# Kernel tuning notes

Measured on AMD Instinct MI355X. Metric: run time of the kernel, lower is better.

Reference implementation:

```python
import jax, jax.numpy as jnp
import numpy as np

D = 128          # fine voxel grid resolution
N0 = 250000
D_IN, D_BASE, D_OUT = 16, 8, 8
EPS = 1e-5
# (cin, cout) for conv0..conv6, conv7, conv9, conv11
_CH = [(16, 8), (8, 16), (16, 16), (16, 32), (32, 32), (32, 64), (64, 64), (64, 32), (32, 16), (16, 8)]

def _offsets():
    r = np.arange(-1, 2)
    return np.stack(np.meshgrid(r, r, r, indexing='ij'), -1).reshape(-1, 3)  # [27,3]

def _lookup_fn(coords, d):
    keys = (coords[:, 0].astype(np.int64) * d + coords[:, 1]) * d + coords[:, 2]
    order = np.argsort(keys)
    skeys = keys[order]
    def lookup(q):
        valid = ((q >= 0) & (q < d)).all(-1)
        k = (q[:, 0].astype(np.int64) * d + q[:, 1]) * d + q[:, 2]
        pos = np.clip(np.searchsorted(skeys, k), 0, len(skeys) - 1)
        return np.where(valid & (skeys[pos] == k), order[pos], -1).astype(np.int32)
    return lookup

def _nbr_same(coords, d):
    # stride-1 sparse conv: outputs at input coords, neighbors at coord+k
    lk = _lookup_fn(coords, d)
    return np.stack([lk(coords + o) for o in _offsets()], 1)  # [N,27]

def _nbr_down(c_out, c_in, d_in):
    # stride-2 conv: output p gathers inputs at 2p+k
    lk = _lookup_fn(c_in, d_in)
    return np.stack([lk(c_out * 2 + o) for o in _offsets()], 1)

def _nbr_up(c_out, c_in, d_in):
    # transposed stride-2 conv: output q gathers input p=(q-k)/2 where divisible
    lk = _lookup_fn(c_in, d_in)
    cols = []
    for o in _offsets():
        q = c_out - o
        div = (q % 2 == 0).all(-1)
        cols.append(np.where(div, lk(q // 2), -1).astype(np.int32))
    return np.stack(cols, 1)

def setup_inputs():
    rng = np.random.default_rng(0)
    flat = rng.choice(D ** 3, size=N0, replace=False)
    c0 = np.stack([flat // (D * D), (flat // D) % D, flat % D], 1).astype(np.int32)
    c1 = np.unique(c0 // 2, axis=0)
    c2 = np.unique(c1 // 2, axis=0)
    c3 = np.unique(c2 // 2, axis=0)
    inp = {
        'feats': jax.random.normal(jax.random.key(0), (N0, D_IN), jnp.float32),
        'nbr0': jnp.asarray(_nbr_same(c0, D)),
        'nbr_d01': jnp.asarray(_nbr_down(c1, c0, D)),
        'nbr1': jnp.asarray(_nbr_same(c1, D // 2)),
        'nbr_d12': jnp.asarray(_nbr_down(c2, c1, D // 2)),
        'nbr2': jnp.asarray(_nbr_same(c2, D // 4)),
        'nbr_d23': jnp.asarray(_nbr_down(c3, c2, D // 4)),
        'nbr3': jnp.asarray(_nbr_same(c3, D // 8)),
        'nbr_u32': jnp.asarray(_nbr_up(c2, c3, D // 8)),
        'nbr_u21': jnp.asarray(_nbr_up(c1, c2, D // 4)),
        'nbr_u10': jnp.asarray(_nbr_up(c0, c1, D // 2)),
    }
    key = jax.random.key(1)
    for i, (ci, co) in enumerate(_CH):
        key, kw = jax.random.split(key)
        inp['w%d' % i] = jax.random.normal(kw, (27, ci, co), jnp.float32) / np.sqrt(27.0 * ci)
        inp['g%d' % i] = jnp.ones((co,), jnp.float32)
        inp['b%d' % i] = jnp.zeros((co,), jnp.float32)
    inp['lin_w'] = jax.random.normal(jax.random.key(2), (D_OUT, D_BASE), jnp.float32) / np.sqrt(D_BASE)
    return inp

def _sconv_bn_relu(f, nbr, w, g, b):
    # f: [Nin,Cin], nbr: [Nout,27] (-1 = no neighbor), w: [27,Cin,Cout]
    gth = jnp.where((nbr >= 0)[..., None], f[jnp.maximum(nbr, 0)], 0.0)  # [Nout,27,Cin]
    y = jnp.einsum('nkc,kco->no', gth, w)
    mu = y.mean(0)                       # training-mode BatchNorm over active voxels
    var = y.var(0)
    return jax.nn.relu((y - mu) * jax.lax.rsqrt(var + EPS) * g + b)

def reference(feats, nbr0, nbr_d01, nbr1, nbr_d12, nbr2, nbr_d23, nbr3, nbr_u32, nbr_u21, nbr_u10,
              w0, g0, b0, w1, g1, b1, w2, g2, b2, w3, g3, b3, w4, g4, b4,
              w5, g5, b5, w6, g6, b6, w7, g7, b7, w8, g8, b8, w9, g9, b9, lin_w):
    c0f = _sconv_bn_relu(feats, nbr0, w0, g0, b0)
    c2f = _sconv_bn_relu(_sconv_bn_relu(c0f, nbr_d01, w1, g1, b1), nbr1, w2, g2, b2)
    c4f = _sconv_bn_relu(_sconv_bn_relu(c2f, nbr_d12, w3, g3, b3), nbr2, w4, g4, b4)
    x = _sconv_bn_relu(_sconv_bn_relu(c4f, nbr_d23, w5, g5, b5), nbr3, w6, g6, b6)
    x = c4f + _sconv_bn_relu(x, nbr_u32, w7, g7, b7)
    x = c2f + _sconv_bn_relu(x, nbr_u21, w8, g8, b8)
    x = c0f + _sconv_bn_relu(x, nbr_u10, w9, g9, b9)
    return x @ lin_w.T, x
```

## Files before the change

### kernel.cpp

```cpp
#include <hip/hip_runtime.h>

#define EPSV 1e-5f
#define NBUCKET 64

typedef __attribute__((ext_vector_type(8))) short short8;
typedef __attribute__((ext_vector_type(4))) float float4v;

static inline int cdiv(int a, int b) { return (a + b - 1) / b; }
static inline int imin(int a, int b) { return a < b ? a : b; }

__device__ inline unsigned short f2bf(float x) {
  unsigned u = __float_as_uint(x);
  return (unsigned short)((u + 0x7FFFu + ((u >> 16) & 1u)) >> 16);
}
__device__ inline float bf2f(unsigned short u) {
  return __uint_as_float(((unsigned)u) << 16);
}

struct PrepArgs {
  const float* w[10];
  unsigned short* wt[10];
  int ci[10];
  int co[10];
  int wcum[11];
  const float* feats;
  unsigned short* featsb;
  int nfeat4;
  float* stats;
};

__global__ __launch_bounds__(256) void prep_kernel(PrepArgs p, long total) {
  const int nstat4 = 10 * NBUCKET * 128 / 4;
  for (long tid0 = (long)blockIdx.x * 256 + threadIdx.x; tid0 < total;
       tid0 += (long)gridDim.x * 256) {
    long tid = tid0;
    if (tid < nstat4) {
      ((float4*)p.stats)[tid] = make_float4(0.f, 0.f, 0.f, 0.f);
      continue;
    }
    tid -= nstat4;
    if (tid < p.nfeat4) {
      float4 v = ((const float4*)p.feats)[tid];
      ushort4 r;
      r.x = f2bf(v.x); r.y = f2bf(v.y); r.z = f2bf(v.z); r.w = f2bf(v.w);
      ((ushort4*)p.featsb)[tid] = r;
      continue;
    }
    tid -= p.nfeat4;
    if (tid >= p.wcum[10]) continue;
    int i = 0;
    while (tid >= p.wcum[i + 1]) ++i;
    int e = (int)(tid - p.wcum[i]);
    int ci = p.ci[i], co = p.co[i];
    int k = e / (ci * co);
    int r = e - k * (ci * co);
    int o = r / ci;
    int c = r - o * ci;
    p.wt[i][((long)k * co + o) * ci + c] = f2bf(p.w[i][((long)k * ci + c) * co + o]);
  }
}

template<int CI, int CO, int MINW>
__global__ __launch_bounds__(256, MINW) void conv_mfma(
    const unsigned short* __restrict__ f, const int* __restrict__ nbr,
    const unsigned short* __restrict__ wt, unsigned short* __restrict__ y,
    float* __restrict__ stats, int nout) {
  constexpr int NCHUNK = (CI == 8) ? 7 : (CI == 16) ? 14 : (CI == 32) ? 27 : 54;
  constexpr int CIP = (CI == 64) ? 64 : (CI == 32) ? 40 : (CI == 16) ? 24 : 12;
  constexpr int RB = (CO < 16) ? CO : 16;
  constexpr bool TWO = (CI <= 16);
  constexpr int NT = TWO ? 2 : 1;

  __shared__ int nbrT[NT * 64 * 27];
  __shared__ unsigned short Bs[27 * RB * CIP];

  const int tid = threadIdx.x;
  const int lane = tid & 63;
  const int wid = tid >> 6;
  const int m = lane & 15;
  const int mm = m & (RB - 1);
  const int quad = lane >> 4;
  const int cbase = blockIdx.y * 16;
  const int co = cbase + m;
  const bool cok = co < CO;

  auto tapof = [&](int c) -> int {
    if constexpr (CI == 8) return c * 4 + quad;
    else if constexpr (CI == 16) return c * 2 + (quad >> 1);
    else if constexpr (CI == 32) return c;
    else return c >> 1;
  };
  auto cioof = [&](int c) -> int {
    if constexpr (CI == 8) return 0;
    else if constexpr (CI == 16) return (quad & 1) * 8;
    else if constexpr (CI == 32) return quad * 8;
    else return ((c & 1) << 5) + quad * 8;
  };
  auto baddr = [&](int tap, int r, int cio) -> int {
    if constexpr (CI == 64) {
      int byt = (tap * 16 + r) * 128 + cio * 2;
      byt ^= (r & 7) << 4;
      return byt >> 1;
    } else {
      return (tap * RB + r) * CIP + cio;
    }
  };

  const int rowb0 = blockIdx.x * (NT * 64);

  {
    constexpr int NC8 = CI / 8;
    for (int t = tid; t < 27 * RB * NC8; t += 256) {
      int tap = t / (RB * NC8);
      int r = t - tap * (RB * NC8);
      int mo = r / NC8;
      int c8 = (r - mo * NC8) * 8;
      short8 v;
#pragma unroll
      for (int q = 0; q < 8; ++q) v[q] = 0;
      int c = cbase + mo;
      if (c < CO) v = *(const short8*)(wt + ((long)tap * CO + c) * CI + c8);
      *(short8*)&Bs[baddr(tap, mo, c8)] = v;
    }
  }
  {
    const long base = (long)rowb0 * 27;
    const long lim = (long)nout * 27;
    for (int j = tid; j < NT * 432; j += 256) {
      long g = base + j * 4;
      int4 v;
      if (g + 4 <= lim) {
        v = *(const int4*)(nbr + g);
      } else {
        v.x = (g + 0 < lim) ? nbr[g + 0] : -1;
        v.y = (g + 1 < lim) ? nbr[g + 1] : -1;
        v.z = (g + 2 < lim) ? nbr[g + 2] : -1;
        v.w = (g + 3 < lim) ? nbr[g + 3] : -1;
      }
      *(int4*)&nbrT[j * 4] = v;
    }
  }
  __syncthreads();

  const int rowb = rowb0 + wid * 16;
  const int lrow = (wid * 16 + m) * 27;
  float sum = 0.f, sq = 0.f;

  if constexpr (TWO) {
    int idx0[NCHUNK], idx1[NCHUNK];
#pragma unroll
    for (int c = 0; c < NCHUNK; ++c) {
      int tap = tapof(c);
      idx0[c] = (tap < 27) ? nbrT[lrow + tap] : -1;
      idx1[c] = (tap < 27) ? nbrT[1728 + lrow + tap] : -1;
    }
    short8 A0[NCHUNK], A1[NCHUNK];
#pragma unroll
    for (int c = 0; c < NCHUNK; ++c) {
      short8 a;
#pragma unroll
      for (int q = 0; q < 8; ++q) a[q] = 0;
      if (idx0[c] >= 0) a = *(const short8*)(f + (long)idx0[c] * CI + cioof(c));
      A0[c] = a;
    }
#pragma unroll
    for (int c = 0; c < NCHUNK; ++c) {
      short8 a;
#pragma unroll
      for (int q = 0; q < 8; ++q) a[q] = 0;
      if (idx1[c] >= 0) a = *(const short8*)(f + (long)idx1[c] * CI + cioof(c));
      A1[c] = a;
    }
    __builtin_amdgcn_sched_barrier(0);
    float4v acc0 = {0.f, 0.f, 0.f, 0.f};
    float4v acc1 = {0.f, 0.f, 0.f, 0.f};
#pragma unroll
    for (int c = 0; c < NCHUNK; ++c) {
      int tap = tapof(c);
      int tapc = tap < 27 ? tap : 26;
      short8 bf = *(const short8*)&Bs[baddr(tapc, mm, cioof(c))];
      acc0 = __builtin_amdgcn_mfma_f32_16x16x32_bf16(A0[c], bf, acc0, 0, 0, 0);
      acc1 = __builtin_amdgcn_mfma_f32_16x16x32_bf16(A1[c], bf, acc1, 0, 0, 0);
    }
#pragma unroll
    for (int r = 0; r < 4; ++r) {
      float v0 = acc0[r];
      int o0 = rowb + quad * 4 + r;
      if (cok && o0 < nout) y[(long)o0 * CO + co] = f2bf(v0);
      sum += v0;
      sq = fmaf(v0, v0, sq);
      float v1 = acc1[r];
      int o1 = rowb + 64 + quad * 4 + r;
      if (cok && o1 < nout) y[(long)o1 * CO + co] = f2bf(v1);
      sum += v1;
      sq = fmaf(v1, v1, sq);
    }
  } else if constexpr (CI == 32) {
    int idxs[27];
#pragma unroll
    for (int t = 0; t < 27; ++t) idxs[t] = nbrT[lrow + t];
    short8 A[27];
#pragma unroll
    for (int c = 0; c < 27; ++c) {
      short8 a;
#pragma unroll
      for (int q = 0; q < 8; ++q) a[q] = 0;
      if (idxs[c] >= 0) a = *(const short8*)(f + (long)idxs[c] * 32 + quad * 8);
      A[c] = a;
    }
    __builtin_amdgcn_sched_barrier(0);
    float4v acc = {0.f, 0.f, 0.f, 0.f};
#pragma unroll
    for (int c = 0; c < 27; ++c) {
      short8 bf = *(const short8*)&Bs[baddr(c, mm, quad * 8)];
      acc = __builtin_amdgcn_mfma_f32_16x16x32_bf16(A[c], bf, acc, 0, 0, 0);
    }
#pragma unroll
    for (int r = 0; r < 4; ++r) {
      float v = acc[r];
      int orow = rowb + quad * 4 + r;
      if (cok && orow < nout) y[(long)orow * CO + co] = f2bf(v);
      sum += v;
      sq = fmaf(v, v, sq);
    }
  } else {
    constexpr int G = 9;
    constexpr int NG = NCHUNK / G;
    short8 A[2][G];
    auto load_group = [&](int g, int bi) {
#pragma unroll
      for (int j = 0; j < G; ++j) {
        const int c = g * G + j;
        const int tap = tapof(c);
        int idx = nbrT[lrow + tap];
        short8 a;
#pragma unroll
        for (int q = 0; q < 8; ++q) a[q] = 0;
        if (idx >= 0) a = *(const short8*)(f + (long)idx * CI + cioof(c));
        A[bi][j] = a;
      }
    };
    float4v acc = {0.f, 0.f, 0.f, 0.f};
    load_group(0, 0);
#pragma unroll
    for (int g = 0; g < NG; ++g) {
      const int cur = g & 1;
      if (g + 1 < NG) load_group(g + 1, cur ^ 1);
#pragma unroll
      for (int j = 0; j < G; ++j) {
        const int c = g * G + j;
        short8 bf = *(const short8*)&Bs[baddr(tapof(c), mm, cioof(c))];
        acc = __builtin_amdgcn_mfma_f32_16x16x32_bf16(A[cur][j], bf, acc, 0, 0, 0);
      }
    }
#pragma unroll
    for (int r = 0; r < 4; ++r) {
      float v = acc[r];
      int orow = rowb + quad * 4 + r;
      if (cok && orow < nout) y[(long)orow * CO + co] = f2bf(v);
      sum += v;
      sq = fmaf(v, v, sq);
    }
  }

  sum += __shfl_xor(sum, 16); sq += __shfl_xor(sq, 16);
  sum += __shfl_xor(sum, 32); sq += __shfl_xor(sq, 32);
  if (quad == 0 && cok) {
    float* st = stats + ((((unsigned)blockIdx.x * 4 + wid) & (NBUCKET - 1)) << 7);
    atomicAdd(&st[co], sum);
    atomicAdd(&st[64 + co], sq);
  }
}

template<int CO>
__global__ __launch_bounds__(256) void bn_relu_bf16(
    const unsigned short* __restrict__ y, const float* __restrict__ stats,
    const float* __restrict__ g, const float* __restrict__ b,
    const unsigned short* __restrict__ skip, unsigned short* __restrict__ out,
    int nout, float inv_n) {
  __shared__ float sA[CO], sC[CO];
  if ((int)threadIdx.x < CO) {
    int o = threadIdx.x;
    float su = 0.f, sq = 0.f;
#pragma unroll 8
    for (int bk = 0; bk < NBUCKET; ++bk) {
      su += stats[bk * 128 + o];
      sq += stats[bk * 128 + 64 + o];
    }
    float mu = su * inv_n;
    float var = sq * inv_n - mu * mu;
    float a = g[o] * rsqrtf(var + EPSV);
    sA[o] = a;
    sC[o] = fmaf(-mu, a, b[o]);
  }
  __syncthreads();
  long total4 = (long)nout * CO / 4;
  for (long i4 = (long)blockIdx.x * 256 + threadIdx.x; i4 < total4;
       i4 += (long)gridDim.x * 256) {
    int o = (int)((i4 * 4) % CO);
    ushort4 v = ((const ushort4*)y)[i4];
    float vv[4] = {bf2f(v.x), bf2f(v.y), bf2f(v.z), bf2f(v.w)};
    unsigned short rr[4];
#pragma unroll
    for (int j = 0; j < 4; ++j) {
      float x = fmaxf(fmaf(vv[j], sA[o + j], sC[o + j]), 0.f);
      if (skip) x += bf2f(skip[i4 * 4 + j]);
      rr[j] = f2bf(x);
    }
    ushort4 r;
    r.x = rr[0]; r.y = rr[1]; r.z = rr[2]; r.w = rr[3];
    ((ushort4*)out)[i4] = r;
  }
}

__global__ __launch_bounds__(256) void tail_kernel(
    const unsigned short* __restrict__ c0f, const float* __restrict__ st9,
    const float* __restrict__ g9, const float* __restrict__ b9, float inv_n,
    const float* __restrict__ lin_w, const unsigned short* __restrict__ y9,
    float* __restrict__ out0, float* __restrict__ x0, int n0) {
  __shared__ float swl[64];
  __shared__ float sbn[16];
  if (threadIdx.x < 64) swl[threadIdx.x] = lin_w[threadIdx.x];
  if (threadIdx.x < 8) {
    int o = threadIdx.x;
    float su = 0.f, sq = 0.f;
#pragma unroll 8
    for (int bk = 0; bk < NBUCKET; ++bk) {
      su += st9[bk * 128 + o];
      sq += st9[bk * 128 + 64 + o];
    }
    float mu = su * inv_n;
    float var = sq * inv_n - mu * mu;
    float a = g9[o] * rsqrtf(var + EPSV);
    sbn[o] = a;
    sbn[8 + o] = fmaf(-mu, a, b9[o]);
  }
  __syncthreads();
  for (int n = blockIdx.x * 256 + (int)threadIdx.x; n < n0; n += gridDim.x * 256) {
    const ushort4* pr = (const ushort4*)(y9 + (long)n * 8);
    ushort4 r0 = pr[0], r1 = pr[1];
    unsigned short rw[8] = {r0.x, r0.y, r0.z, r0.w, r1.x, r1.y, r1.z, r1.w};
    const ushort4* pc = (const ushort4*)(c0f + (long)n * 8);
    ushort4 c0 = pc[0], c1 = pc[1];
    unsigned short cs[8] = {c0.x, c0.y, c0.z, c0.w, c1.x, c1.y, c1.z, c1.w};
    float xv[8];
#pragma unroll
    for (int c = 0; c < 8; ++c)
      xv[c] = bf2f(cs[c]) + fmaxf(fmaf(bf2f(rw[c]), sbn[c], sbn[8 + c]), 0.f);
    *(float4*)(x0 + (long)n * 8) = make_float4(xv[0], xv[1], xv[2], xv[3]);
    *(float4*)(x0 + (long)n * 8 + 4) = make_float4(xv[4], xv[5], xv[6], xv[7]);
    float ov[8];
#pragma unroll
    for (int j = 0; j < 8; ++j) {
      float s = 0.f;
#pragma unroll
      for (int c = 0; c < 8; ++c) s = fmaf(xv[c], swl[j * 8 + c], s);
      ov[j] = s;
    }
    *(float4*)(out0 + (long)n * 8) = make_float4(ov[0], ov[1], ov[2], ov[3]);
    *(float4*)(out0 + (long)n * 8 + 4) = make_float4(ov[4], ov[5], ov[6], ov[7]);
  }
}

extern "C" void kernel_launch(void* const* d_in, const int* in_sizes, int n_in,
                              void* d_out, int out_size, void* d_ws, size_t ws_size,
                              hipStream_t stream) {
  const float* feats   = (const float*)d_in[0];
  const int* nbr0      = (const int*)d_in[1];
  const int* nbr_d01   = (const int*)d_in[2];
  const int* nbr1      = (const int*)d_in[3];
  const int* nbr_d12   = (const int*)d_in[4];
  const int* nbr2      = (const int*)d_in[5];
  const int* nbr_d23   = (const int*)d_in[6];
  const int* nbr3      = (const int*)d_in[7];
  const int* nbr_u32   = (const int*)d_in[8];
  const int* nbr_u21   = (const int*)d_in[9];
  const int* nbr_u10   = (const int*)d_in[10];
  const float* w[10];
  const float* g[10];
  const float* b[10];
  for (int i = 0; i < 10; ++i) {
    w[i] = (const float*)d_in[11 + 3 * i];
    g[i] = (const float*)d_in[12 + 3 * i];
    b[i] = (const float*)d_in[13 + 3 * i];
  }
  const float* lin_w = (const float*)d_in[41];

  const int N0 = in_sizes[0] / 16;
  const int N1 = in_sizes[2] / 27;
  const int N2 = in_sizes[4] / 27;
  const int N3 = in_sizes[6] / 27;
  const float i0 = 1.f / N0, i1 = 1.f / N1, i2 = 1.f / N2, i3 = 1.f / N3;

  static const int CIv[10] = {16, 8, 16, 16, 32, 32, 64, 64, 32, 16};
  static const int COv[10] = {8, 16, 16, 32, 32, 64, 64, 32, 16, 8};

  float* stats = (float*)d_ws;
  unsigned short* u = (unsigned short*)(stats + 10 * NBUCKET * 128);

  unsigned short* yraw = u; u += (size_t)N1 * 32;

  unsigned short* wt[10];
  int wcum[11];
  wcum[0] = 0;
  for (int i = 0; i < 10; ++i) {
    wt[i] = u;
    int sz = 27 * CIv[i] * COv[i];
    u += sz;
    wcum[i + 1] = wcum[i] + sz;
  }
  unsigned short* featsb = u; u += (size_t)N0 * 16;
  unsigned short* c0f = u;    u += (size_t)N0 * 8;
  unsigned short* t1  = u;    u += (size_t)N1 * 16;
  unsigned short* c2f = u;    u += (size_t)N1 * 16;
  unsigned short* t2  = u;    u += (size_t)N2 * 32;
  unsigned short* c4f = u;    u += (size_t)N2 * 32;
  unsigned short* t3  = u;    u += (size_t)N3 * 64;
  unsigned short* t4  = u;    u += (size_t)N3 * 64;
  unsigned short* t5  = t2;
  unsigned short* t6  = t1;
  float* out0 = (float*)d_out;
  float* x0   = (float*)d_out + (size_t)N0 * 8;

  float* s[10];
  for (int i = 0; i < 10; ++i) s[i] = stats + i * NBUCKET * 128;

  PrepArgs pa;
  for (int i = 0; i < 10; ++i) {
    pa.w[i] = w[i]; pa.wt[i] = wt[i];
    pa.ci[i] = CIv[i]; pa.co[i] = COv[i];
    pa.wcum[i] = wcum[i];
  }
  pa.wcum[10] = wcum[10];
  pa.feats = feats; pa.featsb = featsb;
  pa.nfeat4 = N0 * 16 / 4;
  pa.stats = stats;
  long prep_total = (10 * NBUCKET * 128 / 4) + pa.nfeat4 + wcum[10];
  prep_kernel<<<imin((int)((prep_total + 255) / 256), 2048), 256, 0, stream>>>(pa, prep_total);

  auto bgrid = [](long nout, int co) {
    return imin((int)((nout * co / 4 + 255) / 256), 1024);
  };

  int g2_0 = cdiv(N0, 128), g2_1 = cdiv(N1, 128), g2_2 = cdiv(N2, 128);
  int g1_1 = cdiv(N1, 64), g1_2 = cdiv(N2, 64), g1_3 = cdiv(N3, 64);

  conv_mfma<16, 8, 2><<<dim3(g2_0, 1), 256, 0, stream>>>(featsb, nbr0, wt[0], yraw, s[0], N0);
  bn_relu_bf16<8><<<bgrid(N0, 8), 256, 0, stream>>>(yraw, s[0], g[0], b[0], nullptr, c0f, N0, i0);

  conv_mfma<8, 16, 4><<<dim3(g2_1, 1), 256, 0, stream>>>(c0f, nbr_d01, wt[1], yraw, s[1], N1);
  bn_relu_bf16<16><<<bgrid(N1, 16), 256, 0, stream>>>(yraw, s[1], g[1], b[1], nullptr, t1, N1, i1);

  conv_mfma<16, 16, 2><<<dim3(g2_1, 1), 256, 0, stream>>>(t1, nbr1, wt[2], yraw, s[2], N1);
  bn_relu_bf16<16><<<bgrid(N1, 16), 256, 0, stream>>>(yraw, s[2], g[2], b[2], nullptr, c2f, N1, i1);

  conv_mfma<16, 32, 2><<<dim3(g2_2, 2), 256, 0, stream>>>(c2f, nbr_d12, wt[3], yraw, s[3], N2);
  bn_relu_bf16<32><<<bgrid(N2, 32), 256, 0, stream>>>(yraw, s[3], g[3], b[3], nullptr, t2, N2, i2);

  conv_mfma<32, 32, 2><<<dim3(g1_2, 2), 256, 0, stream>>>(t2, nbr2, wt[4], yraw, s[4], N2);
  bn_relu_bf16<32><<<bgrid(N2, 32), 256, 0, stream>>>(yraw, s[4], g[4], b[4], nullptr, c4f, N2, i2);

  conv_mfma<32, 64, 2><<<dim3(g1_3, 4), 256, 0, stream>>>(c4f, nbr_d23, wt[5], yraw, s[5], N3);
  bn_relu_bf16<64><<<bgrid(N3, 64), 256, 0, stream>>>(yraw, s[5], g[5], b[5], nullptr, t3, N3, i3);

  conv_mfma<64, 64, 2><<<dim3(g1_3, 4), 256, 0, stream>>>(t3, nbr3, wt[6], yraw, s[6], N3);
  bn_relu_bf16<64><<<bgrid(N3, 64), 256, 0, stream>>>(yraw, s[6], g[6], b[6], nullptr, t4, N3, i3);

  conv_mfma<64, 32, 2><<<dim3(g1_2, 2), 256, 0, stream>>>(t4, nbr_u32, wt[7], yraw, s[7], N2);
  bn_relu_bf16<32><<<bgrid(N2, 32), 256, 0, stream>>>(yraw, s[7], g[7], b[7], c4f, t5, N2, i2);

  conv_mfma<32, 16, 2><<<dim3(g1_1, 1), 256, 0, stream>>>(t5, nbr_u21, wt[8], yraw, s[8], N1);
  bn_relu_bf16<16><<<bgrid(N1, 16), 256, 0, stream>>>(yraw, s[8], g[8], b[8], c2f, t6, N1, i1);

  conv_mfma<16, 8, 2><<<dim3(g2_0, 1), 256, 0, stream>>>(t6, nbr_u10, wt[9], yraw, s[9], N0);

  tail_kernel<<<imin(cdiv(N0, 256), 1024), 256, 0, stream>>>(
      c0f, s[9], g[9], b[9], i0, lin_w, yraw, out0, x0, N0);
}
```

Measured before the change: 426.7 us.

## Add sparse-list conv kernel that gathers only valid neighbors for sparse layers

Adds a conv_sparse kernel that compacts each wavefront's valid neighbor entries into per-tap-group lists in shared memory, then gathers only those feature rows into a zeroed, swizzled A tile before running the MFMA. It replaces the dense conv_mfma on the level-0 convs, the first downsample and the upsampling convs, where most of the 27 neighbor slots are empty. The goal is to avoid loading and multiplying padding for missing neighbors. In exchange it adds LDS atomics, zero-fill passes per tap group and smaller 64-row blocks.

```diff
diff --git a/kernel.cpp b/kernel.cpp
--- a/kernel.cpp
+++ b/kernel.cpp
@@ -6,8 +6,8 @@
 typedef __attribute__((ext_vector_type(8))) short short8;
 typedef __attribute__((ext_vector_type(4))) float float4v;
 
-static inline int cdiv(int a, int b) { return (a + b - 1) / b; }
-static inline int imin(int a, int b) { return a < b ? a : b; }
+__host__ __device__ static inline int cdiv(int a, int b) { return (a + b - 1) / b; }
+__host__ __device__ static inline int imin(int a, int b) { return a < b ? a : b; }
 
 __device__ inline unsigned short f2bf(float x) {
   unsigned u = __float_as_uint(x);
@@ -57,6 +57,176 @@
     int o = r / ci;
     int c = r - o * ci;
     p.wt[i][((long)k * co + o) * ci + c] = f2bf(p.w[i][((long)k * ci + c) * co + o]);
+  }
+}
+
+template<int CI, int CO>
+__global__ __launch_bounds__(256, 2) void conv_sparse(
+    const unsigned short* __restrict__ f, const int* __restrict__ nbr,
+    const unsigned short* __restrict__ wt, unsigned short* __restrict__ y,
+    float* __restrict__ stats, int nout) {
+  constexpr int NH = CI / 8;
+  constexpr int TK = (CI == 8) ? 27 : (CI == 16) ? 14 : (CI == 32) ? 5 : 3;
+  constexpr int NR = (27 + TK - 1) / TK;
+  constexpr int ASLOT = (CI == 32) ? 20 : (CI == 64) ? 24 : 32;
+  constexpr int SWZ = (CI == 32) ? 3 : 7;
+  constexpr int RB = (CO < 16) ? CO : 16;
+  constexpr int CIP = (CI == 64) ? 64 : (CI == 32) ? 40 : (CI == 16) ? 24 : 12;
+  constexpr int CAP = 16 * TK;
+  constexpr int CPR = (CI == 32) ? 5 : (CI == 64) ? 6 : 7;
+
+  __shared__ unsigned short Bs[27 * RB * CIP];
+  __shared__ short Ash[4][16 * ASLOT * 8];
+  __shared__ unsigned lst[4][NR][CAP];
+  __shared__ int cnt[4][NR];
+
+  const int tid = threadIdx.x;
+  const int lane = tid & 63;
+  const int wid = tid >> 6;
+  const int m = lane & 15;
+  const int mm = m & (RB - 1);
+  const int quad = lane >> 4;
+  const int cbase = blockIdx.y * 16;
+  const int co = cbase + m;
+  const bool cok = co < CO;
+
+  auto baddr = [&](int tap, int r, int cio) -> int {
+    if constexpr (CI == 64) {
+      int byt = (tap * 16 + r) * 128 + cio * 2;
+      byt ^= (r & 7) << 4;
+      return byt >> 1;
+    } else {
+      return (tap * RB + r) * CIP + cio;
+    }
+  };
+
+  const int rowb0 = blockIdx.x * 64;
+  const int rowb = rowb0 + wid * 16;
+
+  {
+    constexpr int NC8 = CI / 8;
+    for (int t = tid; t < 27 * RB * NC8; t += 256) {
+      int tap = t / (RB * NC8);
+      int r = t - tap * (RB * NC8);
+      int mo = r / NC8;
+      int c8 = (r - mo * NC8) * 8;
+      short8 v;
+#pragma unroll
+      for (int q = 0; q < 8; ++q) v[q] = 0;
+      int c = cbase + mo;
+      if (c < CO) v = *(const short8*)(wt + ((long)tap * CO + c) * CI + c8);
+      *(short8*)&Bs[baddr(tap, mo, c8)] = v;
+    }
+  }
+
+  if (lane < NR) cnt[wid][lane] = 0;
+  {
+    const int ve = imin(432, (nout - rowb) * 27);
+    const int* nb = nbr + (long)rowb * 27;
+    for (int k = 0; k < 2; ++k) {
+      int eb = (lane + (k << 6)) << 2;
+      if (eb >= ve) continue;
+      int4 v;
+      if (eb + 4 <= ve) {
+        v = *(const int4*)(nb + eb);
+      } else {
+        v.x = (eb + 0 < ve) ? nb[eb + 0] : -1;
+        v.y = (eb + 1 < ve) ? nb[eb + 1] : -1;
+        v.z = (eb + 2 < ve) ? nb[eb + 2] : -1;
+        v.w = (eb + 3 < ve) ? nb[eb + 3] : -1;
+      }
+      int vv[4] = {v.x, v.y, v.z, v.w};
+#pragma unroll
+      for (int t = 0; t < 4; ++t) {
+        int e = eb + t;
+        int idx = vv[t];
+        if (e < ve && idx >= 0) {
+          int row = e / 27;
+          int tap = e - row * 27;
+          int r = tap / TK;
+          int pos = atomicAdd(&cnt[wid][r], 1);
+          lst[wid][r][pos] = ((unsigned)idx << 9) | ((unsigned)row << 5) | (unsigned)tap;
+        }
+      }
+    }
+  }
+  __syncthreads();
+
+  float4v acc = {0.f, 0.f, 0.f, 0.f};
+
+  for (int r = 0; r < NR; ++r) {
+    for (int t = lane; t < 16 * ASLOT; t += 64) {
+      short8 z;
+#pragma unroll
+      for (int q = 0; q < 8; ++q) z[q] = 0;
+      *(short8*)&Ash[wid][t * 8] = z;
+    }
+    int n = cnt[wid][r];
+    for (int j = lane; j < n * NH; j += 64) {
+      unsigned v = lst[wid][r][j / NH];
+      int h = j & (NH - 1);
+      int idx = (int)(v >> 9);
+      int row = (int)((v >> 5) & 15u);
+      int tap = (int)(v & 31u);
+      short8 a = *(const short8*)(f + (long)idx * CI + h * 8);
+      int slot = (tap - r * TK) * NH + h;
+      int sidx = row * (ASLOT * 8) + (((slot * 8)) ^ ((row & SWZ) << 3));
+      *(short8*)&Ash[wid][sidx] = a;
+    }
+#pragma unroll
+    for (int cc = 0; cc < CPR; ++cc) {
+      int tap, slot, cio;
+      if constexpr (CI == 8) {
+        tap = 4 * cc + quad; slot = tap; cio = 0;
+      } else if constexpr (CI == 16) {
+        int tc = 2 * cc + (quad >> 1);
+        tap = r * 14 + tc; slot = tc * 2 + (quad & 1); cio = (quad & 1) * 8;
+      } else if constexpr (CI == 32) {
+        tap = r * 5 + cc; slot = cc * 4 + quad; cio = quad * 8;
+      } else {
+        tap = r * 3 + (cc >> 1); slot = (cc >> 1) * 8 + (cc & 1) * 4 + quad;
+        cio = (cc & 1) * 32 + quad * 8;
+      }
+      int tapc = tap < 27 ? tap : 26;
+      int sidx = m * (ASLOT * 8) + (((slot * 8)) ^ ((m & SWZ) << 3));
+      short8 av = *(const short8*)&Ash[wid][sidx];
+      short8 bf = *(const short8*)&Bs[baddr(tapc, mm, cio)];
+      acc = __builtin_amdgcn_mfma_f32_16x16x32_bf16(av, bf, acc, 0, 0, 0);
+    }
+  }
+
+  float sum = 0.f, sq = 0.f;
+#pragma unroll
+  for (int rr = 0; rr < 4; ++rr) {
+    float v = acc[rr];
+    sum += v;
+    sq = fmaf(v, v, sq);
+    if (m < RB) Ash[wid][(quad * 4 + rr) * RB + m] = (short)f2bf(v);
+  }
+  if constexpr (RB == 8) {
+    if (lane < 16) {
+      int row = rowb + lane;
+      if (row < nout) {
+        short8 vv = *(const short8*)&Ash[wid][lane * 8];
+        *(short8*)(y + (long)row * CO) = vv;
+      }
+    }
+  } else {
+    if (lane < 32) {
+      int row = rowb + (lane >> 1);
+      if (row < nout) {
+        short8 vv = *(const short8*)&Ash[wid][lane * 8];
+        *(short8*)(y + (long)row * CO + cbase + (lane & 1) * 8) = vv;
+      }
+    }
+  }
+
+  sum += __shfl_xor(sum, 16); sq += __shfl_xor(sq, 16);
+  sum += __shfl_xor(sum, 32); sq += __shfl_xor(sq, 32);
+  if (quad == 0 && cok) {
+    float* st = stats + ((((unsigned)blockIdx.x * 4 + wid) & (NBUCKET - 1)) << 7);
+    atomicAdd(&st[co], sum);
+    atomicAdd(&st[64 + co], sq);
   }
 }
 
@@ -442,13 +612,14 @@
     return imin((int)((nout * co / 4 + 255) / 256), 1024);
   };
 
-  int g2_0 = cdiv(N0, 128), g2_1 = cdiv(N1, 128), g2_2 = cdiv(N2, 128);
-  int g1_1 = cdiv(N1, 64), g1_2 = cdiv(N2, 64), g1_3 = cdiv(N3, 64);
-
-  conv_mfma<16, 8, 2><<<dim3(g2_0, 1), 256, 0, stream>>>(featsb, nbr0, wt[0], yraw, s[0], N0);
+  int tb0 = cdiv(N0, 64), tb1 = cdiv(N1, 64), tb2 = cdiv(N2, 64), tb3 = cdiv(N3, 64);
+  int g2_1 = cdiv(N1, 128), g2_2 = cdiv(N2, 128);
+  int g1_2 = cdiv(N2, 64), g1_3 = cdiv(N3, 64);
+
+  conv_sparse<16, 8><<<dim3(tb0, 1), 256, 0, stream>>>(featsb, nbr0, wt[0], yraw, s[0], N0);
   bn_relu_bf16<8><<<bgrid(N0, 8), 256, 0, stream>>>(yraw, s[0], g[0], b[0], nullptr, c0f, N0, i0);
 
-  conv_mfma<8, 16, 4><<<dim3(g2_1, 1), 256, 0, stream>>>(c0f, nbr_d01, wt[1], yraw, s[1], N1);
+  conv_sparse<8, 16><<<dim3(tb1, 1), 256, 0, stream>>>(c0f, nbr_d01, wt[1], yraw, s[1], N1);
   bn_relu_bf16<16><<<bgrid(N1, 16), 256, 0, stream>>>(yraw, s[1], g[1], b[1], nullptr, t1, N1, i1);
 
   conv_mfma<16, 16, 2><<<dim3(g2_1, 1), 256, 0, stream>>>(t1, nbr1, wt[2], yraw, s[2], N1);
@@ -466,13 +637,13 @@
   conv_mfma<64, 64, 2><<<dim3(g1_3, 4), 256, 0, stream>>>(t3, nbr3, wt[6], yraw, s[6], N3);
   bn_relu_bf16<64><<<bgrid(N3, 64), 256, 0, stream>>>(yraw, s[6], g[6], b[6], nullptr, t4, N3, i3);
 
-  conv_mfma<64, 32, 2><<<dim3(g1_2, 2), 256, 0, stream>>>(t4, nbr_u32, wt[7], yraw, s[7], N2);
+  conv_sparse<64, 32><<<dim3(tb2, 2), 256, 0, stream>>>(t4, nbr_u32, wt[7], yraw, s[7], N2);
   bn_relu_bf16<32><<<bgrid(N2, 32), 256, 0, stream>>>(yraw, s[7], g[7], b[7], c4f, t5, N2, i2);
 
-  conv_mfma<32, 16, 2><<<dim3(g1_1, 1), 256, 0, stream>>>(t5, nbr_u21, wt[8], yraw, s[8], N1);
+  conv_sparse<32, 16><<<dim3(tb1, 1), 256, 0, stream>>>(t5, nbr_u21, wt[8], yraw, s[8], N1);
   bn_relu_bf16<16><<<bgrid(N1, 16), 256, 0, stream>>>(yraw, s[8], g[8], b[8], c2f, t6, N1, i1);
 
-  conv_mfma<16, 8, 2><<<dim3(g2_0, 1), 256, 0, stream>>>(t6, nbr_u10, wt[9], yraw, s[9], N0);
+  conv_sparse<16, 8><<<dim3(tb0, 1), 256, 0, stream>>>(t6, nbr_u10, wt[9], yraw, s[9], N0);
 
   tail_kernel<<<imin(cdiv(N0, 256), 1024), 256, 0, stream>>>(
       c0f, s[9], g[9], b[9], i0, lin_w, yraw, out0, x0, N0);
```

Result: slower. 511.6 us (+19.9%).
